# Kernel tuning notes

Measured on AMD Instinct MI355X. Metric: run time of the kernel, lower is better.

## Reference

```python
import jax, jax.numpy as jnp
import numpy as np

N = 50000      # nodes
E = 800000     # edges (avg degree 16)
LM = 1024      # lm_dim
H = 128        # hidden_channels
OUT = 64       # out_channels


def setup_inputs() -> dict:
    key = jax.random.key(0)
    ks = jax.random.split(key, 13)
    s = 0.02
    return {
        "x": jax.random.normal(ks[0], (N,), dtype=jnp.float32),
        "x_out": jax.random.normal(ks[1], (N, LM), dtype=jnp.float32),
        "c": jax.random.normal(ks[2], (N,), dtype=jnp.float32),
        "edge_index": jax.random.randint(ks[3], (2, E), 0, N, dtype=jnp.int64),
        "edge_weight": jax.random.uniform(ks[4], (E,), dtype=jnp.float32),
        # weights stored as [in, out]
        "Wa": jax.random.normal(ks[5], (1, LM), dtype=jnp.float32) * s,   # aa_linear (no bias)
        "Wc": jax.random.normal(ks[6], (1, LM), dtype=jnp.float32) * s,   # c_linear (no bias)
        "Wl": jax.random.normal(ks[7], (LM, LM), dtype=jnp.float32) * s,  # lm_linear
        "bl": jax.random.normal(ks[8], (LM,), dtype=jnp.float32) * s,
        "W1": jax.random.normal(ks[9], (LM, H), dtype=jnp.float32) * s,   # conv1
        "b1": jax.random.normal(ks[10], (H,), dtype=jnp.float32) * s,
        "W3": jax.random.normal(ks[11], (H, OUT), dtype=jnp.float32) * s,  # conv3
        "b3": jax.random.normal(ks[12], (OUT,), dtype=jnp.float32) * s,
    }


def gcn_conv(h, src, dst, ew, W, b, n):
    """PyG GCNConv with normalize=True, add_self_loops=True."""
    h = h @ W                                   # [n, out]
    loop = jnp.arange(n, dtype=src.dtype)
    src_f = jnp.concatenate([src, loop])
    dst_f = jnp.concatenate([dst, loop])
    ew_f = jnp.concatenate([ew, jnp.ones((n,), ew.dtype)])
    deg = jax.ops.segment_sum(ew_f, dst_f, num_segments=n)     # in-degree incl. self-loops
    dis = jnp.where(deg > 0, jax.lax.rsqrt(deg), 0.0)          # deg^{-1/2}
    norm = dis[src_f] * ew_f * dis[dst_f]                      # per-edge coefficient
    out = jax.ops.segment_sum(norm[:, None] * h[src_f], dst_f, num_segments=n)
    return out + b


def reference(x, x_out, c, edge_index, edge_weight, Wa, Wc, Wl, bl, W1, b1, W3, b3):
    # (c_linear(c[:,None]) + aa_linear(x[:,None]) + lm_linear(x_out)).relu()
    h = jax.nn.relu(c[:, None] * Wc[0] + x[:, None] * Wa[0] + x_out @ Wl + bl)  # [N, LM]
    src, dst = edge_index[0], edge_index[1]
    h = jax.nn.relu(gcn_conv(h, src, dst, edge_weight, W1, b1, N))              # [N, H]
    return gcn_conv(h, src, dst, edge_weight, W3, b3, N)                        # [N, OUT]
```

## Files before the change

### kernel.cpp

```cpp
#include <hip/hip_runtime.h>
#include <hip/hip_bf16.h>

typedef unsigned short u16;
typedef __attribute__((ext_vector_type(8))) short bf16x8;
typedef __attribute__((ext_vector_type(4))) float f32x4;

constexpr int NN = 50000;
constexpr int NE = 800000;
constexpr int LM = 1024;
constexpr int HC = 128;
constexpr int OC = 64;

constexpr size_t OFF_ROWPTR = 0;
constexpr size_t OFF_CURSOR = 200192;
constexpr size_t OFF_COUNTS = 400384;
constexpr size_t OFF_INCL   = 600576;
constexpr size_t OFF_BSUM   = 800768;
constexpr size_t OFF_BOFF   = 801024;
constexpr size_t OFF_DIS    = 801280;
constexpr size_t OFF_META   = 1001472;
constexpr size_t OFF_WLT    = 7401472;
constexpr size_t OFF_W1T    = 9498624;
constexpr size_t OFF_H      = 9760768;
constexpr size_t OFF_Y1     = 112160768;
constexpr size_t OFF_DEGF   = 124960768;
constexpr size_t OFF_Y3     = 137760768;

__device__ __forceinline__ u16 f2bf(float f) {
    union { float f; unsigned int u; } a; a.f = f;
    unsigned int u = a.u + 0x7FFFu + ((a.u >> 16) & 1u);
    return (u16)(u >> 16);
}
__device__ __forceinline__ float bf2f(u16 v) {
    union { unsigned int u; float f; } a; a.u = ((unsigned int)v) << 16;
    return a.f;
}
__device__ __forceinline__ ushort2 pkbf(float a, float b) {
    union { __hip_bfloat162 h; ushort2 u; } cv;
    cv.h = __float22bfloat162_rn(make_float2(a, b));
    return cv.u;
}
__device__ __forceinline__ void async_copy16(u16* lds, const u16* g) {
    __builtin_amdgcn_global_load_lds(
        (const __attribute__((address_space(1))) void*)g,
        (__attribute__((address_space(3))) void*)lds, 16, 0, 0);
}

__global__ void k_setup(int* __restrict__ counts, float* __restrict__ degf,
                        const float* __restrict__ Wl, u16* __restrict__ WlT,
                        const float* __restrict__ W1, u16* __restrict__ W1T) {
    int b = blockIdx.x, t = threadIdx.x;
    if (b < 196) {
        int i = b * 256 + t;
        if (i < NN) { counts[i] = 0; degf[i] = 0.f; }
    } else if (b < 196 + 1024) {
        __shared__ float sm[32][33];
        int bb = b - 196;
        int n0 = (bb & 31) * 32, k0 = (bb >> 5) * 32;
        int ty = t >> 5, tx = t & 31;
        #pragma unroll
        for (int i = 0; i < 4; i++)
            sm[ty + i * 8][tx] = Wl[(size_t)(k0 + ty + i * 8) * LM + n0 + tx];
        __syncthreads();
        #pragma unroll
        for (int i = 0; i < 4; i++)
            WlT[(size_t)(n0 + ty + i * 8) * LM + k0 + tx] = f2bf(sm[tx][ty + i * 8]);
    } else {
        int idx = (b - 1220) * 256 + t;
        if (idx < HC * LM) {
            int o = idx >> 10, k = idx & 1023;
            W1T[idx] = f2bf(W1[(size_t)k * HC + o]);
        }
    }
}

__global__ void k_count(const int* __restrict__ ei, const float* __restrict__ ew,
                        int* __restrict__ counts, float* __restrict__ degf) {
    int e = blockIdx.x * 256 + threadIdx.x;
    if (e < NE) {
        int d = ei[NE + e];
        atomicAdd(&counts[d], 1);
        atomicAdd(&degf[d], ew[e]);
    }
}
__global__ void k_scan1(const int* __restrict__ counts, int* __restrict__ incl,
                        int* __restrict__ bsum) {
    __shared__ int sm[1024];
    int t = threadIdx.x, idx = blockIdx.x * 1024 + t;
    int v = (idx < NN) ? counts[idx] : 0;
    sm[t] = v; __syncthreads();
    for (int off = 1; off < 1024; off <<= 1) {
        int add = (t >= off) ? sm[t - off] : 0;
        __syncthreads();
        sm[t] += add;
        __syncthreads();
    }
    if (idx < NN) incl[idx] = sm[t];
    if (t == 1023) bsum[blockIdx.x] = sm[t];
}
__global__ void k_scan3(const int* __restrict__ incl, const int* __restrict__ counts,
                        const int* __restrict__ bsum, const float* __restrict__ degf,
                        int* __restrict__ rowptr, int* __restrict__ cursor,
                        float* __restrict__ dis) {
    int seg = blockIdx.x >> 2;
    int lane = threadIdx.x & 63;
    int v = (lane < seg) ? bsum[lane] : 0;
    #pragma unroll
    for (int off = 32; off > 0; off >>= 1) v += __shfl_down(v, off, 64);
    int boffv = __shfl(v, 0, 64);
    int idx = blockIdx.x * 256 + threadIdx.x;
    if (idx < NN) {
        int rp = incl[idx] - counts[idx] + boffv;
        rowptr[idx] = rp;
        cursor[idx] = rp;
        dis[idx] = rsqrtf(1.0f + degf[idx]);
    } else if (idx == NN) {
        rowptr[NN] = NE;
    }
}
__global__ void k_fill(const int* __restrict__ ei, const float* __restrict__ ew,
                       const float* __restrict__ dis,
                       int* __restrict__ cursor, int2* __restrict__ meta) {
    int e = blockIdx.x * 256 + threadIdx.x;
    if (e < NE) {
        int s = ei[e];
        int d = ei[NE + e];
        int slot = atomicAdd(&cursor[d], 1);
        meta[slot] = make_int2(s, __float_as_int(ew[e] * dis[s]));
    }
}

__global__ __launch_bounds__(256, 2) void k_gemm1(
    const float* __restrict__ A32, const u16* __restrict__ Bt, u16* __restrict__ Cout,
    const float* __restrict__ xv, const float* __restrict__ cv,
    const float* __restrict__ Wa, const float* __restrict__ Wc,
    const float* __restrict__ bl) {
    __shared__ u16 lA[128 * 64];
    __shared__ u16 lB[2][128 * 64];
    const int tid = threadIdx.x;
    const int lane = tid & 63, wv = tid >> 6;
    const int bx = ((blockIdx.x >> 5) << 3) | (blockIdx.x & 7);
    const int by = (blockIdx.x >> 3) & 3;
    if (bx >= 391) return;
    const int m0 = bx * 128, n0 = by * 256;
    const int wm = (wv >> 1) * 64, wn = (wv & 1) * 64;
    const int fr = lane & 15, qd = lane >> 4;

    f32x4 acc[2][4][4] = {};

    int srl[4], sslot[4]; const float* sbase[4];
    float4 pf[8];
    #pragma unroll
    for (int i = 0; i < 4; i++) {
        int cidx = i * 256 + tid;
        srl[i] = cidx >> 3; sslot[i] = cidx & 7;
        int k8 = sslot[i] ^ (srl[i] & 7);
        int row = m0 + srl[i]; if (row >= NN) row = NN - 1;
        sbase[i] = A32 + (size_t)row * LM + k8 * 8;
    }
    #pragma unroll
    for (int i = 0; i < 4; i++) {
        pf[2 * i]     = *(const float4*)(sbase[i]);
        pf[2 * i + 1] = *(const float4*)(sbase[i] + 4);
    }

    for (int kt = 0; kt < 16; kt++) {
        const int k0 = kt << 6;
        __syncthreads();
        #pragma unroll
        for (int h = 0; h < 2; h++)
            #pragma unroll
            for (int i = 0; i < 4; i++) {
                int r0 = i * 32 + wv * 8;
                int rl = r0 + (lane >> 3);
                int slot = lane & 7;
                int k8 = slot ^ (rl & 7);
                const u16* g = Bt + (size_t)(n0 + h * 128 + rl) * LM + k0 + k8 * 8;
                async_copy16(&lB[h][r0 * 64], g);
            }
        #pragma unroll
        for (int i = 0; i < 4; i++) {
            union { ushort2 u2[4]; bf16x8 v; } pk;
            pk.u2[0] = pkbf(pf[2 * i].x, pf[2 * i].y);
            pk.u2[1] = pkbf(pf[2 * i].z, pf[2 * i].w);
            pk.u2[2] = pkbf(pf[2 * i + 1].x, pf[2 * i + 1].y);
            pk.u2[3] = pkbf(pf[2 * i + 1].z, pf[2 * i + 1].w);
            *(bf16x8*)&lA[srl[i] * 64 + sslot[i] * 8] = pk.v;
        }
        __syncthreads();
        if (kt < 15) {
            #pragma unroll
            for (int i = 0; i < 4; i++) {
                pf[2 * i]     = *(const float4*)(sbase[i] + k0 + 64);
                pf[2 * i + 1] = *(const float4*)(sbase[i] + k0 + 68);
            }
        }
        #pragma unroll
        for (int s = 0; s < 2; s++) {
            const int slot = (s * 4 + qd) ^ (fr & 7);
            bf16x8 af[4];
            #pragma unroll
            for (int mi = 0; mi < 4; mi++)
                af[mi] = *(const bf16x8*)&lA[(wm + mi * 16 + fr) * 64 + slot * 8];
            #pragma unroll
            for (int h = 0; h < 2; h++) {
                bf16x8 bfm[4];
                #pragma unroll
                for (int ni = 0; ni < 4; ni++)
                    bfm[ni] = *(const bf16x8*)&lB[h][(wn + ni * 16 + fr) * 64 + slot * 8];
                #pragma unroll
                for (int mi = 0; mi < 4; mi++)
                    #pragma unroll
                    for (int ni = 0; ni < 4; ni++)
                        acc[h][mi][ni] = __builtin_amdgcn_mfma_f32_16x16x32_bf16(
                            af[mi], bfm[ni], acc[h][mi][ni], 0, 0, 0);
            }
        }
    }

    #pragma unroll
    for (int h = 0; h < 2; h++) {
        int jj[4]; float waj[4], wcj[4], blj[4];
        #pragma unroll
        for (int ni = 0; ni < 4; ni++) {
            jj[ni] = n0 + h * 128 + wn + ni * 16 + fr;
            waj[ni] = Wa[jj[ni]]; wcj[ni] = Wc[jj[ni]]; blj[ni] = bl[jj[ni]];
        }
        #pragma unroll
        for (int mi = 0; mi < 4; mi++)
            #pragma unroll
            for (int r = 0; r < 4; r++) {
                int row = m0 + wm + mi * 16 + qd * 4 + r;
                if (row < NN) {
                    float xb = xv[row], cb = cv[row];
                    #pragma unroll
                    for (int ni = 0; ni < 4; ni++) {
                        float v = acc[h][mi][ni][r] + xb * waj[ni] + cb * wcj[ni] + blj[ni];
                        Cout[(size_t)row * LM + jj[ni]] = f2bf(fmaxf(v, 0.f));
                    }
                }
            }
    }
}

__global__ __launch_bounds__(256) void k_gemm2(
    const u16* __restrict__ Abf, const u16* __restrict__ Bt, u16* __restrict__ Cout) {
    __shared__ u16 lA[64 * 64];
    __shared__ u16 lB[128 * 64];
    const int tid = threadIdx.x;
    const int lane = tid & 63, wv = tid >> 6;
    const int m0 = blockIdx.x * 64;
    const int wm = (wv >> 1) * 32, wn = (wv & 1) * 64;
    const int fr = lane & 15, qd = lane >> 4;
    f32x4 acc[2][4] = {};

    for (int kt = 0; kt < 16; kt++) {
        const int k0 = kt << 6;
        __syncthreads();
        #pragma unroll
        for (int i = 0; i < 4; i++) {
            int r0 = i * 32 + wv * 8;
            int rl = r0 + (lane >> 3);
            int slot = lane & 7;
            int k8 = slot ^ (rl & 7);
            const u16* g = Bt + (size_t)rl * LM + k0 + k8 * 8;
            async_copy16(&lB[r0 * 64], g);
        }
        #pragma unroll
        for (int i = 0; i < 2; i++) {
            int r0 = i * 32 + wv * 8;
            int rl = r0 + (lane >> 3);
            int slot = lane & 7;
            int k8 = slot ^ (rl & 7);
            int row = m0 + rl; if (row >= NN) row = NN - 1;
            const u16* g = Abf + (size_t)row * LM + k0 + k8 * 8;
            async_copy16(&lA[r0 * 64], g);
        }
        __syncthreads();
        #pragma unroll
        for (int s = 0; s < 2; s++) {
            const int slot = (s * 4 + qd) ^ (fr & 7);
            bf16x8 af[2], bfm[4];
            #pragma unroll
            for (int mi = 0; mi < 2; mi++)
                af[mi] = *(const bf16x8*)&lA[(wm + mi * 16 + fr) * 64 + slot * 8];
            #pragma unroll
            for (int ni = 0; ni < 4; ni++)
                bfm[ni] = *(const bf16x8*)&lB[(wn + ni * 16 + fr) * 64 + slot * 8];
            #pragma unroll
            for (int mi = 0; mi < 2; mi++)
                #pragma unroll
                for (int ni = 0; ni < 4; ni++)
                    acc[mi][ni] = __builtin_amdgcn_mfma_f32_16x16x32_bf16(
                        af[mi], bfm[ni], acc[mi][ni], 0, 0, 0);
        }
    }
    #pragma unroll
    for (int mi = 0; mi < 2; mi++)
        #pragma unroll
        for (int r = 0; r < 4; r++) {
            int row = m0 + wm + mi * 16 + qd * 4 + r;
            if (row < NN) {
                #pragma unroll
                for (int ni = 0; ni < 4; ni++)
                    Cout[(size_t)row * HC + wn + ni * 16 + fr] = f2bf(acc[mi][ni][r]);
            }
        }
}

__global__ __launch_bounds__(512) void k_agg1g3(
    const u16* __restrict__ y1, const int* __restrict__ rowptr,
    const int2* __restrict__ meta, const float* __restrict__ dis,
    const float* __restrict__ b1, const float* __restrict__ W3,
    u16* __restrict__ y3) {
    __shared__ float hrow[8][HC];
    int wv = threadIdx.x >> 6, lane = threadIdx.x & 63;
    int node = blockIdx.x * 8 + wv;
    if (node >= NN) return;
    float di = dis[node];
    int p0 = rowptr[node], p1 = rowptr[node + 1];
    ushort2 sv = *(const ushort2*)(y1 + (size_t)node * HC + lane * 2);
    float a0 = di * bf2f(sv.x), a1 = di * bf2f(sv.y);
    #pragma unroll 8
    for (int p = p0; p < p1; ++p) {
        int2 m = meta[p];
        float nm = __int_as_float(m.y);
        ushort2 v = *(const ushort2*)(y1 + (size_t)m.x * HC + lane * 2);
        a0 += nm * bf2f(v.x);
        a1 += nm * bf2f(v.y);
    }
    a0 = fmaxf(di * a0 + b1[lane * 2], 0.f);
    a1 = fmaxf(di * a1 + b1[lane * 2 + 1], 0.f);
    hrow[wv][lane * 2] = a0;
    hrow[wv][lane * 2 + 1] = a1;
    float acc = 0.f;
    #pragma unroll 8
    for (int k = 0; k < HC; ++k)
        acc += hrow[wv][k] * W3[(size_t)k * OC + lane];
    y3[(size_t)node * OC + lane] = f2bf(acc);
}

__global__ __launch_bounds__(256) void k_agg3(
    const u16* __restrict__ y3, const int* __restrict__ rowptr,
    const int2* __restrict__ meta, const float* __restrict__ dis,
    const float* __restrict__ b3, float* __restrict__ outp) {
    int node = blockIdx.x * 4 + (threadIdx.x >> 6);
    int lane = threadIdx.x & 63;
    if (node >= NN) return;
    float di = dis[node];
    int p0 = rowptr[node], p1 = rowptr[node + 1];
    float a = di * bf2f(y3[(size_t)node * OC + lane]);
    #pragma unroll 8
    for (int p = p0; p < p1; ++p) {
        int2 m = meta[p];
        a += __int_as_float(m.y) * bf2f(y3[(size_t)m.x * OC + lane]);
    }
    outp[(size_t)node * OC + lane] = di * a + b3[lane];
}

extern "C" void kernel_launch(void* const* d_in, const int* in_sizes, int n_in,
                              void* d_out, int out_size, void* d_ws, size_t ws_size,
                              hipStream_t stream) {
    const float* x    = (const float*)d_in[0];
    const float* xout = (const float*)d_in[1];
    const float* c    = (const float*)d_in[2];
    const int*   ei   = (const int*)d_in[3];
    const float* ew   = (const float*)d_in[4];
    const float* Wa   = (const float*)d_in[5];
    const float* Wc   = (const float*)d_in[6];
    const float* Wl   = (const float*)d_in[7];
    const float* bl   = (const float*)d_in[8];
    const float* W1   = (const float*)d_in[9];
    const float* b1   = (const float*)d_in[10];
    const float* W3   = (const float*)d_in[11];
    const float* b3   = (const float*)d_in[12];
    float* outp = (float*)d_out;

    char* ws = (char*)d_ws;
    int*   rowptr = (int*)(ws + OFF_ROWPTR);
    int*   cursor = (int*)(ws + OFF_CURSOR);
    int*   counts = (int*)(ws + OFF_COUNTS);
    int*   incl   = (int*)(ws + OFF_INCL);
    int*   bsum   = (int*)(ws + OFF_BSUM);
    float* dis    = (float*)(ws + OFF_DIS);
    int2*  meta   = (int2*)(ws + OFF_META);
    u16*   WlT    = (u16*)(ws + OFF_WLT);
    u16*   W1T    = (u16*)(ws + OFF_W1T);
    u16*   hbuf   = (u16*)(ws + OFF_H);
    u16*   y1     = (u16*)(ws + OFF_Y1);
    float* degf   = (float*)(ws + OFF_DEGF);
    u16*   y3     = (u16*)(ws + OFF_Y3);

    k_setup<<<1732, 256, 0, stream>>>(counts, degf, Wl, WlT, W1, W1T);
    k_count<<<3125, 256, 0, stream>>>(ei, ew, counts, degf);
    k_scan1<<<49, 1024, 0, stream>>>(counts, incl, bsum);
    k_scan3<<<196, 256, 0, stream>>>(incl, counts, bsum, degf, rowptr, cursor, dis);
    k_fill <<<3125, 256, 0, stream>>>(ei, ew, dis, cursor, meta);

    k_gemm1<<<49 * 32, 256, 0, stream>>>(xout, WlT, hbuf, x, c, Wa, Wc, bl);
    k_gemm2<<<782, 256, 0, stream>>>(hbuf, W1T, y1);
    k_agg1g3<<<6250, 512, 0, stream>>>(y1, rowptr, meta, dis, b1, W3, y3);
    k_agg3<<<12500, 256, 0, stream>>>(y3, rowptr, meta, dis, b3, outp);
}
```

Baseline: 707.6 us.

## Pre-convert x_out to bf16 and pack degree count with weight sum atomics

Adds a separate pass that converts the fp32 x_out matrix to bf16 in workspace, and a new GEMM kernel that loads both bf16 operands asynchronously into LDS on 128x128 tiles. It is used only when the workspace is large enough, otherwise the old fused-conversion GEMM runs. The edge counting pass also packs the in-degree count and the fixed-point weighted degree into one 64-bit atomic, replacing two atomics per edge. The trade-off is an extra read and write of the full activation (about 100 MB of bf16) and single-buffered LDS in the new GEMM. The fixed-point weight sum loses a little precision.

```diff
diff --git a/kernel.cpp b/kernel.cpp
--- a/kernel.cpp
+++ b/kernel.cpp
@@ -2,6 +2,7 @@
 #include <hip/hip_bf16.h>
 
 typedef unsigned short u16;
+typedef unsigned long long u64;
 typedef __attribute__((ext_vector_type(8))) short bf16x8;
 typedef __attribute__((ext_vector_type(4))) float f32x4;
 
@@ -13,18 +14,18 @@
 
 constexpr size_t OFF_ROWPTR = 0;
 constexpr size_t OFF_CURSOR = 200192;
-constexpr size_t OFF_COUNTS = 400384;
-constexpr size_t OFF_INCL   = 600576;
-constexpr size_t OFF_BSUM   = 800768;
-constexpr size_t OFF_BOFF   = 801024;
-constexpr size_t OFF_DIS    = 801280;
-constexpr size_t OFF_META   = 1001472;
-constexpr size_t OFF_WLT    = 7401472;
-constexpr size_t OFF_W1T    = 9498624;
-constexpr size_t OFF_H      = 9760768;
-constexpr size_t OFF_Y1     = 112160768;
-constexpr size_t OFF_DEGF   = 124960768;
-constexpr size_t OFF_Y3     = 137760768;
+constexpr size_t OFF_PK     = 400384;
+constexpr size_t OFF_INCL   = 800512;
+constexpr size_t OFF_BSUM   = 1000704;
+constexpr size_t OFF_DIS    = 1000960;
+constexpr size_t OFF_META   = 1201152;
+constexpr size_t OFF_WLT    = 7601408;
+constexpr size_t OFF_W1T    = 9698560;
+constexpr size_t OFF_H      = 9960704;
+constexpr size_t OFF_Y1     = 112360704;
+constexpr size_t OFF_Y3     = 125160704;
+constexpr size_t OFF_ABF    = 131560704;
+constexpr size_t NEED_FAST  = OFF_ABF + (size_t)NN * LM * 2;
 
 __device__ __forceinline__ u16 f2bf(float f) {
     union { float f; unsigned int u; } a; a.f = f;
@@ -46,13 +47,13 @@
         (__attribute__((address_space(3))) void*)lds, 16, 0, 0);
 }
 
-__global__ void k_setup(int* __restrict__ counts, float* __restrict__ degf,
+__global__ void k_setup(u64* __restrict__ pk,
                         const float* __restrict__ Wl, u16* __restrict__ WlT,
                         const float* __restrict__ W1, u16* __restrict__ W1T) {
     int b = blockIdx.x, t = threadIdx.x;
     if (b < 196) {
         int i = b * 256 + t;
-        if (i < NN) { counts[i] = 0; degf[i] = 0.f; }
+        if (i < NN) pk[i] = 0ULL;
     } else if (b < 196 + 1024) {
         __shared__ float sm[32][33];
         int bb = b - 196;
@@ -75,19 +76,19 @@
 }
 
 __global__ void k_count(const int* __restrict__ ei, const float* __restrict__ ew,
-                        int* __restrict__ counts, float* __restrict__ degf) {
+                        u64* __restrict__ pk) {
     int e = blockIdx.x * 256 + threadIdx.x;
     if (e < NE) {
         int d = ei[NE + e];
-        atomicAdd(&counts[d], 1);
-        atomicAdd(&degf[d], ew[e]);
-    }
-}
-__global__ void k_scan1(const int* __restrict__ counts, int* __restrict__ incl,
+        u64 add = (1ULL << 48) | (u64)(ew[e] * 4294967296.0);
+        atomicAdd(&pk[d], add);
+    }
+}
+__global__ void k_scan1(const u64* __restrict__ pk, int* __restrict__ incl,
                         int* __restrict__ bsum) {
     __shared__ int sm[1024];
     int t = threadIdx.x, idx = blockIdx.x * 1024 + t;
-    int v = (idx < NN) ? counts[idx] : 0;
+    int v = (idx < NN) ? (int)(pk[idx] >> 48) : 0;
     sm[t] = v; __syncthreads();
     for (int off = 1; off < 1024; off <<= 1) {
         int add = (t >= off) ? sm[t - off] : 0;
@@ -98,8 +99,8 @@
     if (idx < NN) incl[idx] = sm[t];
     if (t == 1023) bsum[blockIdx.x] = sm[t];
 }
-__global__ void k_scan3(const int* __restrict__ incl, const int* __restrict__ counts,
-                        const int* __restrict__ bsum, const float* __restrict__ degf,
+__global__ void k_scan3(const int* __restrict__ incl, const u64* __restrict__ pk,
+                        const int* __restrict__ bsum,
                         int* __restrict__ rowptr, int* __restrict__ cursor,
                         float* __restrict__ dis) {
     int seg = blockIdx.x >> 2;
@@ -110,10 +111,13 @@
     int boffv = __shfl(v, 0, 64);
     int idx = blockIdx.x * 256 + threadIdx.x;
     if (idx < NN) {
-        int rp = incl[idx] - counts[idx] + boffv;
+        u64 p = pk[idx];
+        int cnt = (int)(p >> 48);
+        float deg = (float)((double)(p & 0xFFFFFFFFFFFFULL) * 2.3283064365386963e-10);
+        int rp = incl[idx] - cnt + boffv;
         rowptr[idx] = rp;
         cursor[idx] = rp;
-        dis[idx] = rsqrtf(1.0f + degf[idx]);
+        dis[idx] = rsqrtf(1.0f + deg);
     } else if (idx == NN) {
         rowptr[NN] = NE;
     }
@@ -130,7 +134,104 @@
     }
 }
 
-__global__ __launch_bounds__(256, 2) void k_gemm1(
+__global__ __launch_bounds__(256) void k_cvtA(const float* __restrict__ A32,
+                                              u16* __restrict__ Abf) {
+    size_t idx = (size_t)blockIdx.x * 256 + threadIdx.x;
+    const float* src = A32 + idx * 8;
+    float4 v0 = *(const float4*)(src);
+    float4 v1 = *(const float4*)(src + 4);
+    union { ushort2 u2[4]; bf16x8 v; } pk;
+    pk.u2[0] = pkbf(v0.x, v0.y);
+    pk.u2[1] = pkbf(v0.z, v0.w);
+    pk.u2[2] = pkbf(v1.x, v1.y);
+    pk.u2[3] = pkbf(v1.z, v1.w);
+    *(bf16x8*)(Abf + idx * 8) = pk.v;
+}
+
+__global__ __launch_bounds__(256, 2) void k_gemm1a(
+    const u16* __restrict__ Abf, const u16* __restrict__ Bt, u16* __restrict__ Cout,
+    const float* __restrict__ xv, const float* __restrict__ cv,
+    const float* __restrict__ Wa, const float* __restrict__ Wc,
+    const float* __restrict__ bl) {
+    __shared__ u16 lA[128 * 64];
+    __shared__ u16 lB[128 * 64];
+    const int tid = threadIdx.x;
+    const int lane = tid & 63, wv = tid >> 6;
+    int x = blockIdx.x & 7, j = blockIdx.x >> 3;
+    int bx = (j & ~7) | x;
+    int by = j & 7;
+    if (bx >= 391) return;
+    const int m0 = bx * 128, n0 = by * 128;
+    const int wm = (wv >> 1) * 64, wn = (wv & 1) * 64;
+    const int fr = lane & 15, qd = lane >> 4;
+
+    f32x4 acc[4][4] = {};
+
+    for (int kt = 0; kt < 16; kt++) {
+        const int k0 = kt << 6;
+        __syncthreads();
+        #pragma unroll
+        for (int i = 0; i < 4; i++) {
+            int r0 = i * 32 + wv * 8;
+            int rl = r0 + (lane >> 3);
+            int slot = lane & 7;
+            int k8 = slot ^ (rl & 7);
+            const u16* g = Bt + (size_t)(n0 + rl) * LM + k0 + k8 * 8;
+            async_copy16(&lB[r0 * 64], g);
+        }
+        #pragma unroll
+        for (int i = 0; i < 4; i++) {
+            int r0 = i * 32 + wv * 8;
+            int rl = r0 + (lane >> 3);
+            int slot = lane & 7;
+            int k8 = slot ^ (rl & 7);
+            int row = m0 + rl; if (row >= NN) row = NN - 1;
+            const u16* g = Abf + (size_t)row * LM + k0 + k8 * 8;
+            async_copy16(&lA[r0 * 64], g);
+        }
+        __syncthreads();
+        #pragma unroll
+        for (int s = 0; s < 2; s++) {
+            const int slot = (s * 4 + qd) ^ (fr & 7);
+            bf16x8 af[4], bfm[4];
+            #pragma unroll
+            for (int mi = 0; mi < 4; mi++)
+                af[mi] = *(const bf16x8*)&lA[(wm + mi * 16 + fr) * 64 + slot * 8];
+            #pragma unroll
+            for (int ni = 0; ni < 4; ni++)
+                bfm[ni] = *(const bf16x8*)&lB[(wn + ni * 16 + fr) * 64 + slot * 8];
+            #pragma unroll
+            for (int mi = 0; mi < 4; mi++)
+                #pragma unroll
+                for (int ni = 0; ni < 4; ni++)
+                    acc[mi][ni] = __builtin_amdgcn_mfma_f32_16x16x32_bf16(
+                        af[mi], bfm[ni], acc[mi][ni], 0, 0, 0);
+        }
+    }
+
+    int jj[4]; float waj[4], wcj[4], blj[4];
+    #pragma unroll
+    for (int ni = 0; ni < 4; ni++) {
+        jj[ni] = n0 + wn + ni * 16 + fr;
+        waj[ni] = Wa[jj[ni]]; wcj[ni] = Wc[jj[ni]]; blj[ni] = bl[jj[ni]];
+    }
+    #pragma unroll
+    for (int mi = 0; mi < 4; mi++)
+        #pragma unroll
+        for (int r = 0; r < 4; r++) {
+            int row = m0 + wm + mi * 16 + qd * 4 + r;
+            if (row < NN) {
+                float xb = xv[row], cb = cv[row];
+                #pragma unroll
+                for (int ni = 0; ni < 4; ni++) {
+                    float v = acc[mi][ni][r] + xb * waj[ni] + cb * wcj[ni] + blj[ni];
+                    Cout[(size_t)row * LM + jj[ni]] = f2bf(fmaxf(v, 0.f));
+                }
+            }
+        }
+}
+
+__global__ __launch_bounds__(256, 2) void k_gemm1f(
     const float* __restrict__ A32, const u16* __restrict__ Bt, u16* __restrict__ Cout,
     const float* __restrict__ xv, const float* __restrict__ cv,
     const float* __restrict__ Wa, const float* __restrict__ Wc,
@@ -379,7 +480,7 @@
     char* ws = (char*)d_ws;
     int*   rowptr = (int*)(ws + OFF_ROWPTR);
     int*   cursor = (int*)(ws + OFF_CURSOR);
-    int*   counts = (int*)(ws + OFF_COUNTS);
+    u64*   pk     = (u64*)(ws + OFF_PK);
     int*   incl   = (int*)(ws + OFF_INCL);
     int*   bsum   = (int*)(ws + OFF_BSUM);
     float* dis    = (float*)(ws + OFF_DIS);
@@ -388,16 +489,21 @@
     u16*   W1T    = (u16*)(ws + OFF_W1T);
     u16*   hbuf   = (u16*)(ws + OFF_H);
     u16*   y1     = (u16*)(ws + OFF_Y1);
-    float* degf   = (float*)(ws + OFF_DEGF);
     u16*   y3     = (u16*)(ws + OFF_Y3);
-
-    k_setup<<<1732, 256, 0, stream>>>(counts, degf, Wl, WlT, W1, W1T);
-    k_count<<<3125, 256, 0, stream>>>(ei, ew, counts, degf);
-    k_scan1<<<49, 1024, 0, stream>>>(counts, incl, bsum);
-    k_scan3<<<196, 256, 0, stream>>>(incl, counts, bsum, degf, rowptr, cursor, dis);
+    u16*   Abf    = (u16*)(ws + OFF_ABF);
+
+    k_setup<<<1732, 256, 0, stream>>>(pk, Wl, WlT, W1, W1T);
+    k_count<<<3125, 256, 0, stream>>>(ei, ew, pk);
+    k_scan1<<<49, 1024, 0, stream>>>(pk, incl, bsum);
+    k_scan3<<<196, 256, 0, stream>>>(incl, pk, bsum, rowptr, cursor, dis);
     k_fill <<<3125, 256, 0, stream>>>(ei, ew, dis, cursor, meta);
 
-    k_gemm1<<<49 * 32, 256, 0, stream>>>(xout, WlT, hbuf, x, c, Wa, Wc, bl);
+    if (ws_size >= NEED_FAST) {
+        k_cvtA  <<<25000, 256, 0, stream>>>(xout, Abf);
+        k_gemm1a<<<392 * 8, 256, 0, stream>>>(Abf, WlT, hbuf, x, c, Wa, Wc, bl);
+    } else {
+        k_gemm1f<<<49 * 32, 256, 0, stream>>>(xout, WlT, hbuf, x, c, Wa, Wc, bl);
+    }
     k_gemm2<<<782, 256, 0, stream>>>(hbuf, W1T, y1);
     k_agg1g3<<<6250, 512, 0, stream>>>(y1, rowptr, meta, dis, b1, W3, y3);
     k_agg3<<<12500, 256, 0, stream>>>(y3, rowptr, meta, dis, b3, outp);
```

Result: faster. 662.7 us (-6.3%).
